# Kernel optimization log

Measured on AMD Instinct MI355X. Metric: run time of the kernel, lower is better.

The kernel has to match this reference:

```python
import jax, jax.numpy as jnp
import numpy as np
from jax import lax

K = 5
C_IN, C_OUT, H, W, N = 256, 128, 270, 480, 512


def setup_inputs() -> dict:
    key = jax.random.key(0)
    ks = jax.random.split(key, 7)
    backbone_map = jax.random.normal(ks[0], (C_IN, H, W), dtype=jnp.float32)
    centers = jax.random.randint(ks[1], (N, 2), 0, 270, dtype=jnp.int32)
    L = jax.random.uniform(ks[2], (N, K), dtype=jnp.float32)
    conv_w = jax.random.normal(ks[3], (C_OUT, C_IN, 3, 3), dtype=jnp.float32) * 0.02
    conv_b = jax.random.normal(ks[4], (C_OUT,), dtype=jnp.float32) * 0.02
    fc_w = jax.random.normal(ks[5], (K, C_OUT), dtype=jnp.float32) * 0.05
    fc_b = jax.random.normal(ks[6], (K,), dtype=jnp.float32) * 0.05
    return {"backbone_map": backbone_map, "centers": centers, "L": L,
            "conv_w": conv_w, "conv_b": conv_b, "fc_w": fc_w, "fc_b": fc_b}


def reference(backbone_map, centers, L, conv_w, conv_b, fc_w, fc_b):
    # 3x3 conv, padding=1, 256 -> 128 channels (unbatched CHW input)
    x = backbone_map[None]  # [1, C_in, H, W]
    E = lax.conv_general_dilated(x, conv_w, window_strides=(1, 1), padding='SAME',
                                 dimension_numbers=('NCHW', 'OIHW', 'NCHW'))[0]
    E = jax.nn.relu(E + conv_b[:, None, None])  # [C_out, H, W]
    # per-object gather: vec_i = E[:, c_y, c_x]  (centers[i] = (c_x, c_y))
    c_x = centers[:, 0]
    c_y = centers[:, 1]
    vecs = E[:, c_y, c_x].T  # [N, C_out]
    logits = vecs @ fc_w.T + fc_b  # [N, K]
    P = jax.nn.softmax(logits, axis=-1)  # softmax over the K-vector per object
    L_identity = -jnp.sum(L * jnp.log(P))
    return P, L_identity
```

## Files before the change

### kernel.cpp

```cpp
#include <hip/hip_runtime.h>

#define C_IN   256
#define C_OUT  128
#define H_DIM  270
#define W_DIM  480
#define N_PTS  512
#define K_CLS  5

#define PB     16
#define CC     32
#define CI_PER (C_IN / CC)
#define TERMS  (CI_PER * 9)
#define JOBS   (PB * CI_PER * 3)
#define WPT    (TERMS / 2)
#define PTG_N  (N_PTS / PB)

__device__ __forceinline__ unsigned short f2bf(float f) {
    unsigned u = __float_as_uint(f);
    return (unsigned short)((u + 0x7FFFu + ((u >> 16) & 1u)) >> 16);
}

__global__ __launch_bounds__(256) void gather_conv(
        const float* __restrict__ bb,
        const int*   __restrict__ centers,
        const float* __restrict__ conv_w,
        float*       __restrict__ part)
{
    __shared__ float          patch[PB][TERMS];
    __shared__ unsigned short w_s[TERMS * C_OUT];

    const int chunk = blockIdx.x & (CC - 1);
    const int ptg   = blockIdx.x >> 5;
    const int t     = threadIdx.x;

    float pv[2][3];
    #pragma unroll
    for (int jj = 0; jj < 2; ++jj) {
        pv[jj][0] = pv[jj][1] = pv[jj][2] = 0.f;
        const int i = t + jj * 256;
        if (i < JOBS) {
            const int pt  = i & 15;
            const int rem = i >> 4;
            const int lci = rem / 3;
            const int dy  = rem - lci * 3;
            const int n   = ptg * PB + pt;
            const int cx  = centers[2 * n];
            const int cy  = centers[2 * n + 1];
            const int y   = cy + dy - 1;
            if (y >= 0 && y < H_DIM) {
                const float* row = bb +
                    ((size_t)(chunk * CI_PER + lci) * H_DIM + y) * W_DIM + cx;
                pv[jj][1] = row[0];
                pv[jj][2] = row[1];
                if (cx >= 1) pv[jj][0] = row[-1];
            }
        }
    }

    const int co   = t >> 1;
    const int half = t & 1;
    const float* wsrc = conv_w + (size_t)co * (C_IN * 9)
                              + chunk * TERMS + half * WPT;
    float4 wreg[WPT / 4];
    #pragma unroll
    for (int j = 0; j < WPT / 4; ++j)
        wreg[j] = *(const float4*)(wsrc + j * 4);

    #pragma unroll
    for (int jj = 0; jj < 2; ++jj) {
        const int i = t + jj * 256;
        if (i < JOBS) {
            const int pt  = i & 15;
            const int rem = i >> 4;
            const int lci = rem / 3;
            const int dy  = rem - lci * 3;
            float* dst = &patch[pt][lci * 9 + dy * 3];
            dst[0] = pv[jj][0]; dst[1] = pv[jj][1]; dst[2] = pv[jj][2];
        }
    }
    #pragma unroll
    for (int j = 0; j < WPT / 4; ++j) {
        const int T = half * WPT + j * 4;
        w_s[(T + 0) * C_OUT + co] = f2bf(wreg[j].x);
        w_s[(T + 1) * C_OUT + co] = f2bf(wreg[j].y);
        w_s[(T + 2) * C_OUT + co] = f2bf(wreg[j].z);
        w_s[(T + 3) * C_OUT + co] = f2bf(wreg[j].w);
    }
    __syncthreads();

    const int cp = t & 63;
    const int q  = t >> 6;

    float acc[4][2] = {{0.f,0.f},{0.f,0.f},{0.f,0.f},{0.f,0.f}};
    for (int g = 0; g < TERMS; g += 4) {
        float wx[4], wy[4];
        #pragma unroll
        for (int i = 0; i < 4; ++i) {
            const unsigned u =
                *(const unsigned*)&w_s[(g + i) * C_OUT + 2 * cp];
            wx[i] = __uint_as_float(u << 16);
            wy[i] = __uint_as_float(u & 0xFFFF0000u);
        }
        #pragma unroll
        for (int p = 0; p < 4; ++p) {
            const float4 pvv = *(const float4*)&patch[q * 4 + p][g];
            acc[p][0] = fmaf(pvv.x, wx[0], acc[p][0]);
            acc[p][1] = fmaf(pvv.x, wy[0], acc[p][1]);
            acc[p][0] = fmaf(pvv.y, wx[1], acc[p][0]);
            acc[p][1] = fmaf(pvv.y, wy[1], acc[p][1]);
            acc[p][0] = fmaf(pvv.z, wx[2], acc[p][0]);
            acc[p][1] = fmaf(pvv.z, wy[2], acc[p][1]);
            acc[p][0] = fmaf(pvv.w, wx[3], acc[p][0]);
            acc[p][1] = fmaf(pvv.w, wy[3], acc[p][1]);
        }
    }

    float* pout = part + ((size_t)chunk * N_PTS + ptg * PB) * C_OUT + 2 * cp;
    #pragma unroll
    for (int p = 0; p < 4; ++p) {
        *(float2*)(pout + (size_t)(q * 4 + p) * C_OUT) =
            make_float2(acc[p][0], acc[p][1]);
    }
}

__global__ __launch_bounds__(64) void head_kernel(
        const float* __restrict__ part,
        const float* __restrict__ conv_b,
        const float* __restrict__ fc_w,
        const float* __restrict__ fc_b,
        const float* __restrict__ L,
        float*       __restrict__ P,
        float*       __restrict__ loss_part)
{
    const int n    = blockIdx.x;
    const int lane = threadIdx.x;

    const float* pc = part + (size_t)n * C_OUT + 2 * lane;
    float vx = 0.f, vy = 0.f;
    #pragma unroll
    for (int c = 0; c < CC; ++c) {
        const float2 pp = *(const float2*)(pc + (size_t)c * N_PTS * C_OUT);
        vx += pp.x; vy += pp.y;
    }
    const float2 cb = *(const float2*)&conv_b[2 * lane];
    vx = fmaxf(vx + cb.x, 0.f);
    vy = fmaxf(vy + cb.y, 0.f);

    float logit[K_CLS];
    #pragma unroll
    for (int k = 0; k < K_CLS; ++k) {
        const float2 w = *(const float2*)&fc_w[k * C_OUT + 2 * lane];
        float p = vx * w.x + vy * w.y;
        #pragma unroll
        for (int off = 32; off > 0; off >>= 1)
            p += __shfl_xor(p, off, 64);
        logit[k] = p + fc_b[k];
    }

    if (lane == 0) {
        float m = logit[0];
        #pragma unroll
        for (int k = 1; k < K_CLS; ++k) m = fmaxf(m, logit[k]);
        float e[K_CLS];
        float s = 0.f;
        #pragma unroll
        for (int k = 0; k < K_CLS; ++k) { e[k] = expf(logit[k] - m); s += e[k]; }
        const float inv  = 1.f / s;
        const float logs = logf(s);
        float lp = 0.f;
        #pragma unroll
        for (int k = 0; k < K_CLS; ++k) {
            P[n * K_CLS + k] = e[k] * inv;
            lp -= L[n * K_CLS + k] * ((logit[k] - m) - logs);
        }
        loss_part[n] = lp;
    }
}

__global__ __launch_bounds__(512) void reduce_loss(
        const float* __restrict__ loss_part, float* __restrict__ out) {
    __shared__ float sh[N_PTS];
    const int t = threadIdx.x;
    sh[t] = loss_part[t];
    __syncthreads();
    for (int s = N_PTS / 2; s > 0; s >>= 1) {
        if (t < s) sh[t] += sh[t + s];
        __syncthreads();
    }
    if (t == 0) out[0] = sh[0];
}

extern "C" void kernel_launch(void* const* d_in, const int* in_sizes, int n_in,
                              void* d_out, int out_size, void* d_ws, size_t ws_size,
                              hipStream_t stream) {
    const float* bb      = (const float*)d_in[0];
    const int*   centers = (const int*)  d_in[1];
    const float* L       = (const float*)d_in[2];
    const float* conv_w  = (const float*)d_in[3];
    const float* conv_b  = (const float*)d_in[4];
    const float* fc_w    = (const float*)d_in[5];
    const float* fc_b    = (const float*)d_in[6];

    float* out = (float*)d_out;

    float* part      = (float*)d_ws;
    float* loss_part = part + (size_t)CC * N_PTS * C_OUT;

    gather_conv<<<PTG_N * CC, 256, 0, stream>>>(bb, centers, conv_w, part);
    head_kernel<<<N_PTS, 64, 0, stream>>>(part, conv_b, fc_w, fc_b, L, out,
                                          loss_part);
    reduce_loss<<<1, N_PTS, 0, stream>>>(loss_part, out + N_PTS * K_CLS);
}
```

Measured before the change: 24.69 us.

## Use bf16 MFMA for gathered conv GEMM and reduce channel chunks to eight

Replaces the scalar FMA inner product over LDS-staged patches and weights with MFMA 16x16x32 bf16 instructions. Weights go straight from global into register fragments, and the patch is written to LDS in MFMA A-fragment layout. The channel split drops from 32 chunks to 8, so there are fewer blocks and fewer partial sums for the head kernel to reduce, but each block does more gathers. Patch values are now rounded to bf16 as well as weights, which adds rounding error.

After: 21.21 us (median of 2 runs). 1.16x faster.

```diff
diff --git a/kernel.cpp b/kernel.cpp
--- a/kernel.cpp
+++ b/kernel.cpp
@@ -8,118 +8,110 @@
 #define K_CLS  5
 
 #define PB     16
-#define CC     32
+#define CC     8
 #define CI_PER (C_IN / CC)
 #define TERMS  (CI_PER * 9)
+#define KSTEPS (TERMS / 32)
 #define JOBS   (PB * CI_PER * 3)
-#define WPT    (TERMS / 2)
 #define PTG_N  (N_PTS / PB)
+
+using f32x4 = __attribute__((ext_vector_type(4))) float;
+using s16x8 = __attribute__((ext_vector_type(8))) short;
 
 __device__ __forceinline__ unsigned short f2bf(float f) {
     unsigned u = __float_as_uint(f);
     return (unsigned short)((u + 0x7FFFu + ((u >> 16) & 1u)) >> 16);
 }
 
-__global__ __launch_bounds__(256) void gather_conv(
+__global__ __launch_bounds__(256) void gemm_conv(
         const float* __restrict__ bb,
         const int*   __restrict__ centers,
         const float* __restrict__ conv_w,
         float*       __restrict__ part)
 {
-    __shared__ float          patch[PB][TERMS];
-    __shared__ unsigned short w_s[TERMS * C_OUT];
+    __shared__ unsigned short pa[KSTEPS * 64 * 8];
 
     const int chunk = blockIdx.x & (CC - 1);
-    const int ptg   = blockIdx.x >> 5;
+    const int ptg   = blockIdx.x >> 3;
     const int t     = threadIdx.x;
-
-    float pv[2][3];
-    #pragma unroll
-    for (int jj = 0; jj < 2; ++jj) {
-        pv[jj][0] = pv[jj][1] = pv[jj][2] = 0.f;
-        const int i = t + jj * 256;
-        if (i < JOBS) {
-            const int pt  = i & 15;
-            const int rem = i >> 4;
-            const int lci = rem / 3;
-            const int dy  = rem - lci * 3;
-            const int n   = ptg * PB + pt;
-            const int cx  = centers[2 * n];
-            const int cy  = centers[2 * n + 1];
-            const int y   = cy + dy - 1;
-            if (y >= 0 && y < H_DIM) {
-                const float* row = bb +
-                    ((size_t)(chunk * CI_PER + lci) * H_DIM + y) * W_DIM + cx;
-                pv[jj][1] = row[0];
-                pv[jj][2] = row[1];
-                if (cx >= 1) pv[jj][0] = row[-1];
-            }
-        }
-    }
-
-    const int co   = t >> 1;
-    const int half = t & 1;
-    const float* wsrc = conv_w + (size_t)co * (C_IN * 9)
-                              + chunk * TERMS + half * WPT;
-    float4 wreg[WPT / 4];
-    #pragma unroll
-    for (int j = 0; j < WPT / 4; ++j)
-        wreg[j] = *(const float4*)(wsrc + j * 4);
-
-    #pragma unroll
-    for (int jj = 0; jj < 2; ++jj) {
-        const int i = t + jj * 256;
-        if (i < JOBS) {
-            const int pt  = i & 15;
-            const int rem = i >> 4;
-            const int lci = rem / 3;
-            const int dy  = rem - lci * 3;
-            float* dst = &patch[pt][lci * 9 + dy * 3];
-            dst[0] = pv[jj][0]; dst[1] = pv[jj][1]; dst[2] = pv[jj][2];
-        }
-    }
-    #pragma unroll
-    for (int j = 0; j < WPT / 4; ++j) {
-        const int T = half * WPT + j * 4;
-        w_s[(T + 0) * C_OUT + co] = f2bf(wreg[j].x);
-        w_s[(T + 1) * C_OUT + co] = f2bf(wreg[j].y);
-        w_s[(T + 2) * C_OUT + co] = f2bf(wreg[j].z);
-        w_s[(T + 3) * C_OUT + co] = f2bf(wreg[j].w);
+    const int l     = t & 63;
+    const int w     = t >> 6;
+    const int c     = l & 15;
+    const int hi    = l >> 4;
+
+    float pvv[6][3];
+    #pragma unroll
+    for (int jj = 0; jj < 6; ++jj) {
+        const int i   = t + jj * 256;
+        const int pt  = i & 15;
+        const int rem = i >> 4;
+        const int lci = rem / 3;
+        const int dy  = rem - lci * 3;
+        const int n   = ptg * PB + pt;
+        const int cx  = centers[2 * n];
+        const int cy  = centers[2 * n + 1];
+        const int y   = cy + dy - 1;
+        pvv[jj][0] = pvv[jj][1] = pvv[jj][2] = 0.f;
+        if (y >= 0 && y < H_DIM) {
+            const float* row = bb +
+                ((size_t)(chunk * CI_PER + lci) * H_DIM + y) * W_DIM + cx;
+            pvv[jj][1] = row[0];
+            pvv[jj][2] = row[1];
+            if (cx >= 1) pvv[jj][0] = row[-1];
+        }
+    }
+
+    s16x8 bfrag[2][KSTEPS];
+    #pragma unroll
+    for (int ct = 0; ct < 2; ++ct) {
+        const int co = (2 * w + ct) * 16 + c;
+        const float* base = conv_w + (size_t)co * (C_IN * 9)
+                                   + chunk * TERMS + hi * 8;
+        #pragma unroll
+        for (int ks = 0; ks < KSTEPS; ++ks) {
+            const float4 lo = *(const float4*)(base + ks * 32);
+            const float4 hh = *(const float4*)(base + ks * 32 + 4);
+            s16x8 v;
+            v[0] = (short)f2bf(lo.x); v[1] = (short)f2bf(lo.y);
+            v[2] = (short)f2bf(lo.z); v[3] = (short)f2bf(lo.w);
+            v[4] = (short)f2bf(hh.x); v[5] = (short)f2bf(hh.y);
+            v[6] = (short)f2bf(hh.z); v[7] = (short)f2bf(hh.w);
+            bfrag[ct][ks] = v;
+        }
+    }
+
+    #pragma unroll
+    for (int jj = 0; jj < 6; ++jj) {
+        const int i   = t + jj * 256;
+        const int pt  = i & 15;
+        const int rem = i >> 4;
+        const int lci = rem / 3;
+        const int dy  = rem - lci * 3;
+        #pragma unroll
+        for (int dx = 0; dx < 3; ++dx) {
+            const int K  = lci * 9 + dy * 3 + dx;
+            const int ks = K >> 5, r = K & 31;
+            pa[(ks * 64 + (r >> 3) * 16 + pt) * 8 + (r & 7)] =
+                f2bf(pvv[jj][dx]);
+        }
     }
     __syncthreads();
 
-    const int cp = t & 63;
-    const int q  = t >> 6;
-
-    float acc[4][2] = {{0.f,0.f},{0.f,0.f},{0.f,0.f},{0.f,0.f}};
-    for (int g = 0; g < TERMS; g += 4) {
-        float wx[4], wy[4];
-        #pragma unroll
-        for (int i = 0; i < 4; ++i) {
-            const unsigned u =
-                *(const unsigned*)&w_s[(g + i) * C_OUT + 2 * cp];
-            wx[i] = __uint_as_float(u << 16);
-            wy[i] = __uint_as_float(u & 0xFFFF0000u);
-        }
-        #pragma unroll
-        for (int p = 0; p < 4; ++p) {
-            const float4 pvv = *(const float4*)&patch[q * 4 + p][g];
-            acc[p][0] = fmaf(pvv.x, wx[0], acc[p][0]);
-            acc[p][1] = fmaf(pvv.x, wy[0], acc[p][1]);
-            acc[p][0] = fmaf(pvv.y, wx[1], acc[p][0]);
-            acc[p][1] = fmaf(pvv.y, wy[1], acc[p][1]);
-            acc[p][0] = fmaf(pvv.z, wx[2], acc[p][0]);
-            acc[p][1] = fmaf(pvv.z, wy[2], acc[p][1]);
-            acc[p][0] = fmaf(pvv.w, wx[3], acc[p][0]);
-            acc[p][1] = fmaf(pvv.w, wy[3], acc[p][1]);
-        }
-    }
-
-    float* pout = part + ((size_t)chunk * N_PTS + ptg * PB) * C_OUT + 2 * cp;
-    #pragma unroll
-    for (int p = 0; p < 4; ++p) {
-        *(float2*)(pout + (size_t)(q * 4 + p) * C_OUT) =
-            make_float2(acc[p][0], acc[p][1]);
+    f32x4 acc0 = {0.f, 0.f, 0.f, 0.f};
+    f32x4 acc1 = {0.f, 0.f, 0.f, 0.f};
+    #pragma unroll
+    for (int ks = 0; ks < KSTEPS; ++ks) {
+        const s16x8 a = *(const s16x8*)&pa[(ks * 64 + l) * 8];
+        acc0 = __builtin_amdgcn_mfma_f32_16x16x32_bf16(a, bfrag[0][ks], acc0, 0, 0, 0);
+        acc1 = __builtin_amdgcn_mfma_f32_16x16x32_bf16(a, bfrag[1][ks], acc1, 0, 0, 0);
+    }
+
+    #pragma unroll
+    for (int reg = 0; reg < 4; ++reg) {
+        const int n = ptg * PB + hi * 4 + reg;
+        float* pr = part + ((size_t)chunk * N_PTS + n) * C_OUT;
+        pr[(2 * w + 0) * 16 + c] = acc0[reg];
+        pr[(2 * w + 1) * 16 + c] = acc1[reg];
     }
 }
 
@@ -138,8 +130,8 @@
     const float* pc = part + (size_t)n * C_OUT + 2 * lane;
     float vx = 0.f, vy = 0.f;
     #pragma unroll
-    for (int c = 0; c < CC; ++c) {
-        const float2 pp = *(const float2*)(pc + (size_t)c * N_PTS * C_OUT);
+    for (int cidx = 0; cidx < CC; ++cidx) {
+        const float2 pp = *(const float2*)(pc + (size_t)cidx * N_PTS * C_OUT);
         vx += pp.x; vy += pp.y;
     }
     const float2 cb = *(const float2*)&conv_b[2 * lane];
@@ -149,8 +141,8 @@
     float logit[K_CLS];
     #pragma unroll
     for (int k = 0; k < K_CLS; ++k) {
-        const float2 w = *(const float2*)&fc_w[k * C_OUT + 2 * lane];
-        float p = vx * w.x + vy * w.y;
+        const float2 wv = *(const float2*)&fc_w[k * C_OUT + 2 * lane];
+        float p = vx * wv.x + vy * wv.y;
         #pragma unroll
         for (int off = 32; off > 0; off >>= 1)
             p += __shfl_xor(p, off, 64);
@@ -206,7 +198,7 @@
     float* part      = (float*)d_ws;
     float* loss_part = part + (size_t)CC * N_PTS * C_OUT;
 
-    gather_conv<<<PTG_N * CC, 256, 0, stream>>>(bb, centers, conv_w, part);
+    gemm_conv<<<PTG_N * CC, 256, 0, stream>>>(bb, centers, conv_w, part);
     head_kernel<<<N_PTS, 64, 0, stream>>>(part, conv_b, fc_w, fc_b, L, out,
                                           loss_part);
     reduce_loss<<<1, N_PTS, 0, stream>>>(loss_part, out + N_PTS * K_CLS);
```
